# Kernel tuning notes

Hardware: AMD Instinct MI355X
Metric: run time of the kernel (lower is better)

## Reference

```python
import math
import jax, jax.numpy as jnp
import numpy as np

B, S, D, H, FF, N, V, C = 32, 512, 512, 8, 2048, 6, 32000, 16
EPS = 1e-6


def setup_inputs() -> dict:
    key = jax.random.key(0)
    c = [0]
    def w(shape, scale=0.02):
        c[0] += 1
        return jax.random.normal(jax.random.fold_in(key, c[0]), shape, jnp.float32) * scale
    inp = {}
    inp['src_emb'] = w((V, D)).at[0].set(0.0)  # padding_idx=0 row zeroed
    inp['tgt_emb'] = w((C, D)).at[0].set(0.0)
    for p in ['e', 'd', 's']:  # encoder self / decoder self / decoder cross attn
        for nm in ['wq', 'wk', 'wv', 'wo']:
            inp[f'{p}_{nm}'] = w((N, D, D))
            inp[f'{p}_{nm.replace("w", "b")}'] = w((N, D))
    for p in ['e', 'd']:
        inp[f'{p}_w1'] = w((N, D, FF)); inp[f'{p}_b1'] = w((N, FF))
        inp[f'{p}_w2'] = w((N, FF, D)); inp[f'{p}_b2'] = w((N, D))
    inp['gen_w'] = w((D * C, C)); inp['gen_b'] = w((C,))
    inp['scr_x'] = jax.random.randint(jax.random.fold_in(key, 999), (B, S), 0, V, dtype=jnp.int32)
    return inp


def _layernorm(x):
    # torch source: (x - mean) / (std + eps), std is unbiased (ddof=1); gamma=1, beta=0
    m = x.mean(-1, keepdims=True)
    s = jnp.std(x, axis=-1, keepdims=True, ddof=1)
    return (x - m) / (s + EPS)


def _mha(xq, xkv, wq, bq, wk, bk, wv, bv, wo, bo):
    b, lq, _ = xq.shape
    lk = xkv.shape[1]
    dk = D // H
    q = (xq @ wq + bq).reshape(b, lq, H, dk)
    k = (xkv @ wk + bk).reshape(b, lk, H, dk)
    v = (xkv @ wv + bv).reshape(b, lk, H, dk)
    scores = jnp.einsum('bqhd,bkhd->bhqk', q, k) / math.sqrt(dk)
    p = jax.nn.softmax(scores, axis=-1)
    o = jnp.einsum('bhqk,bkhd->bqhd', p, v).reshape(b, lq, D)
    return o @ wo + bo


def _ffn(x, w1, b1, w2, b2):
    return jax.nn.relu(x @ w1 + b1) @ w2 + b2


def _pos_encoding(L):
    pos = jnp.arange(L, dtype=jnp.float32)[:, None]
    div = jnp.exp(jnp.arange(0, D, 2, dtype=jnp.float32) * (-math.log(10000.0) / D))
    pe = jnp.zeros((L, D), jnp.float32)
    pe = pe.at[:, 0::2].set(jnp.sin(pos * div))
    pe = pe.at[:, 1::2].set(jnp.cos(pos * div))
    return pe


def reference(src_emb, tgt_emb,
              e_wq, e_bq, e_wk, e_bk, e_wv, e_bv, e_wo, e_bo, e_w1, e_b1, e_w2, e_b2,
              d_wq, d_bq, d_wk, d_bk, d_wv, d_bv, d_wo, d_bo,
              s_wq, s_bq, s_wk, s_bk, s_wv, s_bv, s_wo, s_bo,
              d_w1, d_b1, d_w2, d_b2, gen_w, gen_b, scr_x):
    sqrt_d = math.sqrt(D)
    # encoder
    x = src_emb[scr_x] * sqrt_d + _pos_encoding(S)[None]
    for i in range(N):
        t = _layernorm(x)
        x = x + _mha(t, t, e_wq[i], e_bq[i], e_wk[i], e_bk[i], e_wv[i], e_bv[i], e_wo[i], e_bo[i])
        t = _layernorm(x)
        x = x + _ffn(t, e_w1[i], e_b1[i], e_w2[i], e_b2[i])
    enc = _layernorm(x)
    # decoder over classify targets arange(C), repeated over batch
    y = jnp.broadcast_to(tgt_emb * sqrt_d + _pos_encoding(C), (B, C, D))
    for i in range(N):
        t = _layernorm(y)
        y = y + _mha(t, t, d_wq[i], d_bq[i], d_wk[i], d_bk[i], d_wv[i], d_bv[i], d_wo[i], d_bo[i])
        t = _layernorm(y)
        y = y + _mha(t, enc, s_wq[i], s_bq[i], s_wk[i], s_bk[i], s_wv[i], s_bv[i], s_wo[i], s_bo[i])
        t = _layernorm(y)
        y = y + _ffn(t, d_w1[i], d_b1[i], d_w2[i], d_b2[i])
    dec = _layernorm(y)
    logits = dec.reshape(B, -1) @ gen_w + gen_b
    return jax.nn.log_softmax(logits, axis=-1)
```

## Files before the change

kernel.cpp:

```cpp
#include <hip/hip_runtime.h>
#include <math.h>

#define NB  32
#define SS  512
#define DD  512
#define HH  8
#define FFD 2048
#define NLAY 6
#define CC  16
#define SQRTD 22.627416997969522f

typedef unsigned short u16;
typedef __attribute__((ext_vector_type(8))) short short8;
typedef __attribute__((ext_vector_type(8))) unsigned short u16x8;
typedef __attribute__((ext_vector_type(4))) float f32x4;

__device__ __forceinline__ u16 f2bf(float f) {
  unsigned u = __builtin_bit_cast(unsigned, f);
  u += 0x7fff + ((u >> 16) & 1);
  return (u16)(u >> 16);
}
__device__ __forceinline__ float bf2f(u16 u) {
  unsigned v = ((unsigned)u) << 16;
  return __builtin_bit_cast(float, v);
}
__device__ __forceinline__ void async16(const u16* g, u16* l) {
  __builtin_amdgcn_global_load_lds(
      (const __attribute__((address_space(1))) unsigned int*)g,
      (__attribute__((address_space(3))) unsigned int*)l, 16, 0, 0);
}
__device__ __forceinline__ int swz(int row, int slice) {
  return row * 128 + ((slice ^ (row & 7)) << 4);
}
__device__ __forceinline__ int vswz(int row, int slice) {
  return row * 128 + ((slice ^ (row & 7) ^ ((row >> 4) & 3)) << 4);
}

__device__ __forceinline__ float pe_val(int pos, int d) {
  int j = d >> 1;
  float freq = expf((float)j * -0.03597789207f);
  float ang = (float)pos * freq;
  return (d & 1) ? cosf(ang) : sinf(ang);
}

__global__ __launch_bounds__(512) void k_embed_src(
    const float* __restrict__ emb, const int* __restrict__ ids,
    float* __restrict__ x) {
  int tok = blockIdx.x;
  int d = threadIdx.x;
  int s = tok & (SS - 1);
  int id = ids[tok];
  x[(size_t)tok * DD + d] = emb[(size_t)id * DD + d] * SQRTD + pe_val(s, d);
}

__global__ __launch_bounds__(512) void k_embed_tgt(
    const float* __restrict__ emb, float* __restrict__ y) {
  int tok = blockIdx.x;
  int d = threadIdx.x;
  int c = tok & (CC - 1);
  y[(size_t)tok * DD + d] = emb[(size_t)c * DD + d] * SQRTD + pe_val(c, d);
}

template <typename OT>
__global__ __launch_bounds__(256) void k_layernorm(
    const float* __restrict__ X, OT* __restrict__ Y) {
  int row = blockIdx.x;
  int tid = threadIdx.x;
  int lane = tid & 63, wv = tid >> 6;
  const float* x = X + (size_t)row * DD;
  float2 v = *(const float2*)(x + tid * 2);
  float s = v.x + v.y;
  #pragma unroll
  for (int off = 32; off; off >>= 1) s += __shfl_xor(s, off);
  __shared__ float red[4];
  if (lane == 0) red[wv] = s;
  __syncthreads();
  float mean = (red[0] + red[1] + red[2] + red[3]) * (1.0f / DD);
  float dx = v.x - mean, dy = v.y - mean;
  float sq = dx * dx + dy * dy;
  #pragma unroll
  for (int off = 32; off; off >>= 1) sq += __shfl_xor(sq, off);
  __syncthreads();
  if (lane == 0) red[wv] = sq;
  __syncthreads();
  float var = (red[0] + red[1] + red[2] + red[3]) * (1.0f / (DD - 1));
  float inv = 1.0f / (sqrtf(var) + 1e-6f);
  float ox = dx * inv, oy = dy * inv;
  if constexpr (sizeof(OT) == 2) {
    ushort2 o; o.x = f2bf(ox); o.y = f2bf(oy);
    *(ushort2*)((u16*)Y + (size_t)row * DD + tid * 2) = o;
  } else {
    float2 o; o.x = ox; o.y = oy;
    *(float2*)((float*)Y + (size_t)row * DD + tid * 2) = o;
  }
}

__global__ __launch_bounds__(256) void k_wt(
    const float* __restrict__ in, u16* __restrict__ out, int K, int N,
    size_t ldl, int roff) {
  __shared__ float tile[32][33];
  const float* ip = in + (size_t)blockIdx.z * K * N;
  u16* op = out + (size_t)blockIdx.z * ldl;
  int n0 = blockIdx.x * 32, k0 = blockIdx.y * 32;
  int tx = threadIdx.x, ty = threadIdx.y;
  #pragma unroll
  for (int i = 0; i < 32; i += 8)
    tile[ty + i][tx] = ip[(size_t)(k0 + ty + i) * N + n0 + tx];
  __syncthreads();
  #pragma unroll
  for (int i = 0; i < 32; i += 8)
    op[(size_t)(roff + n0 + ty + i) * K + k0 + tx] = f2bf(tile[tx][ty + i]);
}

__global__ void k_bcat(const float* __restrict__ b0, const float* __restrict__ b1,
                       const float* __restrict__ b2, float* __restrict__ out,
                       int n0, int n1, int n2) {
  int lay = blockIdx.x, nt = n0 + n1 + n2;
  for (int t = threadIdx.x; t < nt; t += blockDim.x) {
    float v;
    if (t < n0) v = b0[(size_t)lay * n0 + t];
    else if (t < n0 + n1) v = b1[(size_t)lay * n1 + t - n0];
    else v = b2[(size_t)lay * n2 + t - n0 - n1];
    out[(size_t)lay * nt + t] = v;
  }
}

template <typename OT, bool RELU, bool RES, int NT>
__global__ __launch_bounds__(256) void k_mgemm(
    const u16* __restrict__ A, const u16* __restrict__ Bt,
    const float* __restrict__ bias, const float* __restrict__ res,
    OT* __restrict__ C, int M, int N, int K) {
  constexpr int MI = (NT == 128) ? 4 : 2;
  __shared__ u16 As[2][128 * 32];
  __shared__ u16 Bs[2][NT * 32];
  int nbn = N / NT;
  int cpx = gridDim.x >> 3;
  int bid = (blockIdx.x & 7) * cpx + (blockIdx.x >> 3);
  int bm = bid / nbn, bn = bid % nbn;
  int tid = threadIdx.x;
  int wid = tid >> 6, lane = tid & 63;
  int i0 = 2 * wid, i1 = 2 * wid + 1;
  int r0 = 16 * i0 + (lane >> 2), r1 = 16 * i1 + (lane >> 2);
  int kof = (lane & 3) * 8;
  const u16* Ag0 = A + (size_t)(bm * 128 + r0) * K + kof;
  const u16* Ag1 = A + (size_t)(bm * 128 + r1) * K + kof;
  const u16* Bg0;
  const u16* Bg1 = nullptr;
  if constexpr (NT == 128) {
    Bg0 = Bt + (size_t)(bn * 128 + r0) * K + kof;
    Bg1 = Bt + (size_t)(bn * 128 + r1) * K + kof;
  } else {
    int rb = 16 * wid + (lane >> 2);
    Bg0 = Bt + (size_t)(bn * 64 + rb) * K + kof;
  }
  f32x4 acc[MI][4] = {};
  int wm = wid >> 1, wn = wid & 1;
  int aoff, boff;
  if constexpr (NT == 128) {
    aoff = (wm * 64 + (lane & 15)) * 32 + (lane >> 4) * 8;
    boff = (wn * 64 + (lane & 15)) * 32 + (lane >> 4) * 8;
  } else {
    aoff = (wid * 32 + (lane & 15)) * 32 + (lane >> 4) * 8;
    boff = (lane & 15) * 32 + (lane >> 4) * 8;
  }

  auto stage = [&](int buf, int kel) {
    async16(Ag0 + kel, &As[buf][i0 * 512]);
    async16(Ag1 + kel, &As[buf][i1 * 512]);
    if constexpr (NT == 128) {
      async16(Bg0 + kel, &Bs[buf][i0 * 512]);
      async16(Bg1 + kel, &Bs[buf][i1 * 512]);
    } else {
      async16(Bg0 + kel, &Bs[buf][wid * 512]);
    }
  };

  stage(0, 0);
  __syncthreads();
  int nkt = K >> 5;
  for (int kt = 0; kt < nkt; ++kt) {
    int cur = kt & 1;
    if (kt + 1 < nkt) stage(cur ^ 1, (kt + 1) << 5);
    short8 af[MI], bfr[4];
    #pragma unroll
    for (int i = 0; i < MI; ++i)
      af[i] = *(const short8*)&As[cur][aoff + i * 16 * 32];
    #pragma unroll
    for (int i = 0; i < 4; ++i)
      bfr[i] = *(const short8*)&Bs[cur][boff + i * 16 * 32];
    #pragma unroll
    for (int mi = 0; mi < MI; ++mi)
      #pragma unroll
      for (int ni = 0; ni < 4; ++ni)
        acc[mi][ni] = __builtin_amdgcn_mfma_f32_16x16x32_bf16(
            af[mi], bfr[ni], acc[mi][ni], 0, 0, 0);
    __syncthreads();
  }

  int colb, rowb;
  if constexpr (NT == 128) {
    colb = bn * 128 + wn * 64 + (lane & 15);
    rowb = bm * 128 + wm * 64 + ((lane >> 4) << 2);
  } else {
    colb = bn * 64 + (lane & 15);
    rowb = bm * 128 + wid * 32 + ((lane >> 4) << 2);
  }
  #pragma unroll
  for (int mi = 0; mi < MI; ++mi)
    #pragma unroll
    for (int ni = 0; ni < 4; ++ni) {
      int col = colb + ni * 16;
      float bv = bias[col];
      #pragma unroll
      for (int r = 0; r < 4; ++r) {
        int row = rowb + mi * 16 + r;
        float v = acc[mi][ni][r] + bv;
        if constexpr (RES) v += res[(size_t)row * N + col];
        if constexpr (RELU) v = fmaxf(v, 0.f);
        if constexpr (sizeof(OT) == 2) ((u16*)C)[(size_t)row * N + col] = f2bf(v);
        else ((float*)C)[(size_t)row * N + col] = v;
      }
    }
}

__global__ __launch_bounds__(256) void k_attn3(
    const u16* __restrict__ Q, const u16* __restrict__ K,
    const u16* __restrict__ V, u16* __restrict__ O,
    int Lq, int Lk, int nqt, int ldq, int ldk, int ldv, int ldo) {
  __shared__ u16 Qs[64 * 64];
  __shared__ u16 Ks[64 * 64];
  __shared__ u16 VsT[64 * 64];
  __shared__ u16 Ps[64 * 64];
  int cpx = gridDim.x >> 3;
  int bid = (blockIdx.x & 7) * cpx + (blockIdx.x >> 3);
  int qt = bid % nqt;
  int bh = bid / nqt;
  int b = bh >> 3, h = bh & 7;
  int tid = threadIdx.x;
  int wv = tid >> 6, lane = tid & 63;
  int l16 = lane & 15, l4 = lane >> 4;
  int sr = tid >> 2;
  int sc2 = (tid & 3) << 1;

  {
    int qr = qt * 64 + sr;
    const u16* g = Q + (size_t)((size_t)b * Lq + qr) * ldq + h * 64 + (sc2 << 3);
    u16x8 v0 = *(const u16x8*)g;
    u16x8 v1 = *(const u16x8*)(g + 8);
    *(u16x8*)((char*)Qs + swz(sr, sc2)) = v0;
    *(u16x8*)((char*)Qs + swz(sr, sc2 + 1)) = v1;
  }

  f32x4 o_acc[4] = {};
  float l_r[4] = {0.f, 0.f, 0.f, 0.f};
  int qrow = wv * 16 + l16;

  int nkt = Lk >> 6;
  for (int kt = 0; kt < nkt; ++kt) {
    __syncthreads();
    {
      int kr = kt * 64 + sr;
      const u16* gk = K + (size_t)((size_t)b * Lk + kr) * ldk + h * 64 + (sc2 << 3);
      const u16* gv = V + (size_t)((size_t)b * Lk + kr) * ldv + h * 64 + (sc2 << 3);
      u16x8 k0 = *(const u16x8*)gk;
      u16x8 k1 = *(const u16x8*)(gk + 8);
      u16x8 vv0 = *(const u16x8*)gv;
      u16x8 vv1 = *(const u16x8*)(gv + 8);
      *(u16x8*)((char*)Ks + swz(sr, sc2)) = k0;
      *(u16x8*)((char*)Ks + swz(sr, sc2 + 1)) = k1;
      bool oddr = sr & 1;
      u16x8 send = oddr ? vv0 : vv1;
      int4 si = __builtin_bit_cast(int4, send);
      int4 ri;
      ri.x = __shfl_xor(si.x, 4); ri.y = __shfl_xor(si.y, 4);
      ri.z = __shfl_xor(si.z, 4); ri.w = __shfl_xor(si.w, 4);
      u16x8 recv = __builtin_bit_cast(u16x8, ri);
      int colbyte = (sr & 6) << 1;
      int slice = sr >> 3;
      int dbase = (sc2 << 3) + (oddr ? 8 : 0);
      #pragma unroll
      for (int j = 0; j < 8; ++j) {
        u16 lo = oddr ? recv[j] : vv0[j];
        u16 hi = oddr ? vv1[j] : recv[j];
        *(unsigned*)((char*)VsT + vswz(dbase + j, slice) + colbyte) =
            (unsigned)lo | ((unsigned)hi << 16);
      }
    }
    __syncthreads();

    short8 aQ0 = *(const short8*)((char*)Qs + swz(qrow, l4));
    short8 aQ1 = *(const short8*)((char*)Qs + swz(qrow, 4 + l4));
    f32x4 s_acc[4];
    #pragma unroll
    for (int ni = 0; ni < 4; ++ni) {
      int krow = ni * 16 + l16;
      short8 b0 = *(const short8*)((char*)Ks + swz(krow, l4));
      short8 b1 = *(const short8*)((char*)Ks + swz(krow, 4 + l4));
      f32x4 z = {};
      z = __builtin_amdgcn_mfma_f32_16x16x32_bf16(aQ0, b0, z, 0, 0, 0);
      z = __builtin_amdgcn_mfma_f32_16x16x32_bf16(aQ1, b1, z, 0, 0, 0);
      s_acc[ni] = z;
    }

    #pragma unroll
    for (int r = 0; r < 4; ++r) {
      int prow = wv * 16 + l4 * 4 + r;
      #pragma unroll
      for (int ni = 0; ni < 4; ++ni) {
        float p = __expf(s_acc[ni][r] * 0.125f);
        l_r[r] += p;
        int e = ni * 16 + l16;
        ((u16*)((char*)Ps + swz(prow, e >> 3)))[e & 7] = f2bf(p);
      }
    }

    short8 aP0 = *(const short8*)((char*)Ps + swz(qrow, l4));
    short8 aP1 = *(const short8*)((char*)Ps + swz(qrow, 4 + l4));
    #pragma unroll
    for (int ni = 0; ni < 4; ++ni) {
      int vrow = ni * 16 + l16;
      short8 b0 = *(const short8*)((char*)VsT + vswz(vrow, l4));
      short8 b1 = *(const short8*)((char*)VsT + vswz(vrow, 4 + l4));
      o_acc[ni] = __builtin_amdgcn_mfma_f32_16x16x32_bf16(aP0, b0, o_acc[ni], 0, 0, 0);
      o_acc[ni] = __builtin_amdgcn_mfma_f32_16x16x32_bf16(aP1, b1, o_acc[ni], 0, 0, 0);
    }
  }

  #pragma unroll
  for (int r = 0; r < 4; ++r)
    #pragma unroll
    for (int off = 8; off; off >>= 1) l_r[r] += __shfl_xor(l_r[r], off);

  #pragma unroll
  for (int r = 0; r < 4; ++r) {
    int q = qt * 64 + wv * 16 + l4 * 4 + r;
    float inv = 1.0f / l_r[r];
    u16* op = O + (size_t)((size_t)b * Lq + q) * ldo + h * 64 + l16;
    #pragma unroll
    for (int ni = 0; ni < 4; ++ni)
      op[ni * 16] = f2bf(o_acc[ni][r] * inv);
  }
}

__global__ __launch_bounds__(256) void k_attn4(
    const u16* __restrict__ Q, const u16* __restrict__ K,
    const u16* __restrict__ V, u16* __restrict__ O,
    int Lk, int ldq, int ldk, int ldv, int ldo) {
  __shared__ u16 Qs[16 * 64];
  __shared__ u16 Ks[4][64 * 64];
  __shared__ u16 VsT[4][64 * 64];
  __shared__ u16 Ps[4][16 * 64];
  int cpx = gridDim.x >> 3;
  int bid = (blockIdx.x & 7) * cpx + (blockIdx.x >> 3);
  int b = bid >> 3, h = bid & 7;
  int tid = threadIdx.x;
  int wv = tid >> 6, lane = tid & 63;
  int l16 = lane & 15, l4 = lane >> 4;

  if (tid < 64) {
    int qr = tid >> 2;
    int sc2 = (tid & 3) << 1;
    const u16* g = Q + (size_t)((size_t)b * CC + qr) * ldq + h * 64 + (sc2 << 3);
    u16x8 v0 = *(const u16x8*)g;
    u16x8 v1 = *(const u16x8*)(g + 8);
    *(u16x8*)((char*)Qs + swz(qr, sc2)) = v0;
    *(u16x8*)((char*)Qs + swz(qr, sc2 + 1)) = v1;
  }
  __syncthreads();

  u16* KsW = Ks[wv];
  u16* VsW = VsT[wv];
  u16* PsW = Ps[wv];

  f32x4 o_acc[4] = {};
  float l_r[4] = {0.f, 0.f, 0.f, 0.f};

  int nkt = (Lk + 63) >> 6;
  for (int kt = wv; kt < nkt; kt += 4) {
    int kr = kt * 64 + lane; if (kr >= Lk) kr = Lk - 1;
    const u16* gk = K + (size_t)((size_t)b * Lk + kr) * ldk + h * 64;
    const u16* gv = V + (size_t)((size_t)b * Lk + kr) * ldv + h * 64;
    u16x8 vvv[8];
    #pragma unroll
    for (int c = 0; c < 8; ++c) {
      u16x8 kk = *(const u16x8*)(gk + c * 8);
      *(u16x8*)((char*)KsW + swz(lane, c)) = kk;
      vvv[c] = *(const u16x8*)(gv + c * 8);
    }
    bool oddr = lane & 1;
    int4 s0 = __builtin_bit_cast(int4, oddr ? vvv[0] : vvv[4]);
    int4 s1 = __builtin_bit_cast(int4, oddr ? vvv[1] : vvv[5]);
    int4 s2 = __builtin_bit_cast(int4, oddr ? vvv[2] : vvv[6]);
    int4 s3 = __builtin_bit_cast(int4, oddr ? vvv[3] : vvv[7]);
    int4 r0, r1, r2, r3;
    r0.x = __shfl_xor(s0.x, 1); r0.y = __shfl_xor(s0.y, 1);
    r0.z = __shfl_xor(s0.z, 1); r0.w = __shfl_xor(s0.w, 1);
    r1.x = __shfl_xor(s1.x, 1); r1.y = __shfl_xor(s1.y, 1);
    r1.z = __shfl_xor(s1.z, 1); r1.w = __shfl_xor(s1.w, 1);
    r2.x = __shfl_xor(s2.x, 1); r2.y = __shfl_xor(s2.y, 1);
    r2.z = __shfl_xor(s2.z, 1); r2.w = __shfl_xor(s2.w, 1);
    r3.x = __shfl_xor(s3.x, 1); r3.y = __shfl_xor(s3.y, 1);
    r3.z = __shfl_xor(s3.z, 1); r3.w = __shfl_xor(s3.w, 1);
    u16x8 rcv[4] = {
      __builtin_bit_cast(u16x8, r0), __builtin_bit_cast(u16x8, r1),
      __builtin_bit_cast(u16x8, r2), __builtin_bit_cast(u16x8, r3)};
    int colbyte = (lane & 6) << 1;
    int slice = lane >> 3;
    int dbase = oddr ? 32 : 0;
    #pragma unroll
    for (int c = 0; c < 4; ++c)
      #pragma unroll
      for (int j = 0; j < 8; ++j) {
        int d = dbase + c * 8 + j;
        u16 lo = oddr ? rcv[c][j] : vvv[c][j];
        u16 hi = oddr ? vvv[4 + c][j] : rcv[c][j];
        *(unsigned*)((char*)VsW + vswz(d, slice) + colbyte) =
            (unsigned)lo | ((unsigned)hi << 16);
      }

    short8 aQ0 = *(const short8*)((char*)Qs + swz(l16, l4));
    short8 aQ1 = *(const short8*)((char*)Qs + swz(l16, 4 + l4));
    f32x4 s_acc[4];
    __builtin_amdgcn_s_setprio(1);
    #pragma unroll
    for (int ni = 0; ni < 4; ++ni) {
      int krow = ni * 16 + l16;
      short8 b0 = *(const short8*)((char*)KsW + swz(krow, l4));
      short8 b1 = *(const short8*)((char*)KsW + swz(krow, 4 + l4));
      f32x4 z = {};
      z = __builtin_amdgcn_mfma_f32_16x16x32_bf16(aQ0, b0, z, 0, 0, 0);
      z = __builtin_amdgcn_mfma_f32_16x16x32_bf16(aQ1, b1, z, 0, 0, 0);
      s_acc[ni] = z;
    }
    __builtin_amdgcn_s_setprio(0);

    #pragma unroll
    for (int r = 0; r < 4; ++r) {
      int prow = l4 * 4 + r;
      #pragma unroll
      for (int ni = 0; ni < 4; ++ni) {
        int kg = kt * 64 + ni * 16 + l16;
        float p = (kg < Lk) ? __expf(s_acc[ni][r] * 0.125f) : 0.f;
        l_r[r] += p;
        int e = ni * 16 + l16;
        ((u16*)((char*)PsW + swz(prow, e >> 3)))[e & 7] = f2bf(p);
      }
    }

    short8 aP0 = *(const short8*)((char*)PsW + swz(l16, l4));
    short8 aP1 = *(const short8*)((char*)PsW + swz(l16, 4 + l4));
    __builtin_amdgcn_s_setprio(1);
    #pragma unroll
    for (int ni = 0; ni < 4; ++ni) {
      int vrow = ni * 16 + l16;
      short8 b0 = *(const short8*)((char*)VsW + vswz(vrow, l4));
      short8 b1 = *(const short8*)((char*)VsW + vswz(vrow, 4 + l4));
      o_acc[ni] = __builtin_amdgcn_mfma_f32_16x16x32_bf16(aP0, b0, o_acc[ni], 0, 0, 0);
      o_acc[ni] = __builtin_amdgcn_mfma_f32_16x16x32_bf16(aP1, b1, o_acc[ni], 0, 0, 0);
    }
    __builtin_amdgcn_s_setprio(0);
  }

  #pragma unroll
  for (int r = 0; r < 4; ++r)
    #pragma unroll
    for (int off = 8; off; off >>= 1) l_r[r] += __shfl_xor(l_r[r], off);

  float* cO = (float*)KsW;
  float* cL = (float*)VsW;
  #pragma unroll
  for (int r = 0; r < 4; ++r) {
    int q = l4 * 4 + r;
    if (l16 == 0) cL[q] = l_r[r];
    #pragma unroll
    for (int ni = 0; ni < 4; ++ni)
      cO[q * 64 + ni * 16 + l16] = o_acc[ni][r];
  }
  __syncthreads();

  #pragma unroll
  for (int i = 0; i < 4; ++i) {
    int e = tid + 256 * i;
    int q = e >> 6, d = e & 63;
    float den = 0.f, num = 0.f;
    #pragma unroll
    for (int w = 0; w < 4; ++w) {
      den += ((float*)VsT[w])[q];
      num += ((float*)Ks[w])[q * 64 + d];
    }
    O[(size_t)((size_t)b * CC + q) * ldo + h * 64 + d] = f2bf(num / den);
  }
}

__global__ __launch_bounds__(256) void k_gen(
    const float* __restrict__ dec, const float* __restrict__ Wg,
    const float* __restrict__ bg, float* __restrict__ out) {
  int b = blockIdx.x;
  int t = threadIdx.x;
  int n = t & 15, ch = t >> 4;
  const float* a = dec + (size_t)b * (CC * DD);
  float p = 0.f;
  int k0 = ch * 512;
  for (int kk = k0; kk < k0 + 512; ++kk) p += a[kk] * Wg[(size_t)kk * CC + n];
  __shared__ float red[16][17];
  red[ch][n] = p;
  __syncthreads();
  __shared__ float ls[16];
  __shared__ float mm[2];
  if (t < 16) {
    float sv = bg[t];
    #pragma unroll
    for (int jj = 0; jj < 16; ++jj) sv += red[jj][t];
    ls[t] = sv;
  }
  __syncthreads();
  if (t == 0) {
    float m = ls[0];
    for (int jj = 1; jj < 16; ++jj) m = fmaxf(m, ls[jj]);
    float se = 0.f;
    for (int jj = 0; jj < 16; ++jj) se += expf(ls[jj] - m);
    mm[0] = m; mm[1] = logf(se);
  }
  __syncthreads();
  if (t < 16) out[(size_t)b * CC + t] = ls[t] - mm[0] - mm[1];
}

extern "C" void kernel_launch(void* const* d_in, const int* in_sizes, int n_in,
                              void* d_out, int out_size, void* d_ws, size_t ws_size,
                              hipStream_t stream) {
  (void)in_sizes; (void)n_in; (void)out_size; (void)ws_size;
  const float* src_emb = (const float*)d_in[0];
  const float* tgt_emb = (const float*)d_in[1];
  const float* e_wq = (const float*)d_in[2];
  const float* e_bq = (const float*)d_in[3];
  const float* e_wk = (const float*)d_in[4];
  const float* e_bk = (const float*)d_in[5];
  const float* e_wv = (const float*)d_in[6];
  const float* e_bv = (const float*)d_in[7];
  const float* e_wo = (const float*)d_in[8];
  const float* e_bo = (const float*)d_in[9];
  const float* d_wq = (const float*)d_in[10];
  const float* d_bq = (const float*)d_in[11];
  const float* d_wk = (const float*)d_in[12];
  const float* d_bk = (const float*)d_in[13];
  const float* d_wv = (const float*)d_in[14];
  const float* d_bv = (const float*)d_in[15];
  const float* d_wo = (const float*)d_in[16];
  const float* d_bo = (const float*)d_in[17];
  const float* s_wq = (const float*)d_in[18];
  const float* s_bq = (const float*)d_in[19];
  const float* s_wk = (const float*)d_in[20];
  const float* s_bk = (const float*)d_in[21];
  const float* s_wv = (const float*)d_in[22];
  const float* s_bv = (const float*)d_in[23];
  const float* s_wo = (const float*)d_in[24];
  const float* s_bo = (const float*)d_in[25];
  const float* e_w1 = (const float*)d_in[26];
  const float* e_b1 = (const float*)d_in[27];
  const float* e_w2 = (const float*)d_in[28];
  const float* e_b2 = (const float*)d_in[29];
  const float* dw1  = (const float*)d_in[30];
  const float* db1  = (const float*)d_in[31];
  const float* dw2  = (const float*)d_in[32];
  const float* db2  = (const float*)d_in[33];
  const float* gen_w = (const float*)d_in[34];
  const float* gen_b = (const float*)d_in[35];
  const int*   scr   = (const int*)d_in[36];

  float* ws = (float*)d_ws;
  const size_t NBS = (size_t)NB * SS * DD;
  const size_t BCD = (size_t)NB * CC * DD;
  float* x    = ws;
  u16*  t_bf  = (u16*)(ws + NBS);
  u16*  enc_bf = t_bf;
  float* dsm  = ws + NBS + NBS / 2;
  float* dy   = dsm;
  float* tdf  = dsm + BCD;
  u16*  td_bf = (u16*)(tdf + BCD);
  u16*  aod_bf = td_bf + BCD;
  u16*  dqkv_act = aod_bf + BCD;
  u16*  middd_bf = dqkv_act + 3 * BCD;
  u16*  eqkv_act = (u16*)(ws + 2 * NBS);
  u16*  midd_e   = eqkv_act;
  u16*  kv_big   = eqkv_act;
  u16*  kv_x     = (u16*)x;
  u16* wp = (u16*)(ws + 4 * NBS);
  const size_t SQKV = (size_t)NLAY * 1536 * 512;
  const size_t SDD  = (size_t)NLAY * 512 * 512;
  const size_t SKV  = (size_t)NLAY * 1024 * 512;
  const size_t SFF  = (size_t)NLAY * 2048 * 512;
  u16* eqkv_t = wp;            wp += SQKV;
  u16* ewo_t  = wp;            wp += SDD;
  u16* ew1_t  = wp;            wp += SFF;
  u16* ew2_t  = wp;            wp += SFF;
  u16* dqkv_t = wp;            wp += SQKV;
  u16* dwo_t  = wp;            wp += SDD;
  u16* sq_t   = wp;            wp += SDD;
  u16* skv_t  = wp;            wp += SKV;
  u16* swo_t  = wp;            wp += SDD;
  u16* dw1_t  = wp;            wp += SFF;
  u16* dw2_t  = wp;            wp += SFF;
  float* ebqkv = (float*)wp;
  float* dbqkv = ebqkv + NLAY * 1536;
  float* sbkv  = dbqkv + NLAY * 1536;

  const int BS = NB * SS;
  const int BC = NB * CC;

  auto wt = [&](const float* in, u16* out, int K, int N, size_t ldl, int roff) {
    k_wt<<<dim3(N / 32, K / 32, NLAY), dim3(32, 8), 0, stream>>>(in, out, K, N, ldl, roff);
  };
  auto mg = [&](const u16* A, const u16* Bt, const float* bias,
                const float* res, void* C, int M, int N, int K, int relu, int obf) {
    int g128 = (M / 128) * (N / 128);
    if (g128 >= 1024) {
      dim3 g(g128);
      if (obf) {
        if (relu) k_mgemm<u16, true, false, 128><<<g, 256, 0, stream>>>(A, Bt, bias, nullptr, (u16*)C, M, N, K);
        else      k_mgemm<u16, false, false, 128><<<g, 256, 0, stream>>>(A, Bt, bias, nullptr, (u16*)C, M, N, K);
      } else {
        if (res)  k_mgemm<float, false, true, 128><<<g, 256, 0, stream>>>(A, Bt, bias, res, (float*)C, M, N, K);
        else      k_mgemm<float, false, false, 128><<<g, 256, 0, stream>>>(A, Bt, bias, nullptr, (float*)C, M, N, K);
      }
    } else {
      dim3 g((M / 128) * (N / 64));
      if (obf) {
        if (relu) k_mgemm<u16, true, false, 64><<<g, 256, 0, stream>>>(A, Bt, bias, nullptr, (u16*)C, M, N, K);
        else      k_mgemm<u16, false, false, 64><<<g, 256, 0, stream>>>(A, Bt, bias, nullptr, (u16*)C, M, N, K);
      } else {
        if (res)  k_mgemm<float, false, true, 64><<<g, 256, 0, stream>>>(A, Bt, bias, res, (float*)C, M, N, K);
        else      k_mgemm<float, false, false, 64><<<g, 256, 0, stream>>>(A, Bt, bias, nullptr, (float*)C, M, N, K);
      }
    }
  };

  wt(e_wq, eqkv_t, 512, 512, 1536 * 512, 0);
  wt(e_wk, eqkv_t, 512, 512, 1536 * 512, 512);
  wt(e_wv, eqkv_t, 512, 512, 1536 * 512, 1024);
  wt(e_wo, ewo_t,  512, 512, 512 * 512, 0);
  wt(e_w1, ew1_t,  512, 2048, 2048 * 512, 0);
  wt(e_w2, ew2_t,  2048, 512, (size_t)512 * 2048, 0);
  wt(d_wq, dqkv_t, 512, 512, 1536 * 512, 0);
  wt(d_wk, dqkv_t, 512, 512, 1536 * 512, 512);
  wt(d_wv, dqkv_t, 512, 512, 1536 * 512, 1024);
  wt(d_wo, dwo_t,  512, 512, 512 * 512, 0);
  wt(s_wq, sq_t,   512, 512, 512 * 512, 0);
  wt(s_wk, skv_t,  512, 512, 1024 * 512, 0);
  wt(s_wv, skv_t,  512, 512, 1024 * 512, 512);
  wt(s_wo, swo_t,  512, 512, 512 * 512, 0);
  wt(dw1,  dw1_t,  512, 2048, 2048 * 512, 0);
  wt(dw2,  dw2_t,  2048, 512, (size_t)512 * 2048, 0);
  k_bcat<<<NLAY, 512, 0, stream>>>(e_bq, e_bk, e_bv, ebqkv, 512, 512, 512);
  k_bcat<<<NLAY, 512, 0, stream>>>(d_bq, d_bk, d_bv, dbqkv, 512, 512, 512);
  k_bcat<<<NLAY, 512, 0, stream>>>(s_bk, s_bv, s_bv, sbkv, 512, 512, 0);

  k_embed_src<<<BS, 512, 0, stream>>>(src_emb, scr, x);
  for (int i = 0; i < NLAY; ++i) {
    size_t bo = (size_t)i * DD, b1o = (size_t)i * FFD;
    k_layernorm<u16><<<BS, 256, 0, stream>>>(x, t_bf);
    mg(t_bf, eqkv_t + (size_t)i * 1536 * 512, ebqkv + i * 1536, nullptr,
       eqkv_act, BS, 1536, 512, 0, 1);
    k_attn3<<<NB * HH * (SS / 64), 256, 0, stream>>>(
        eqkv_act, eqkv_act + 512, eqkv_act + 1024, t_bf,
        SS, SS, SS / 64, 1536, 1536, 1536, 512);
    mg(t_bf, ewo_t + (size_t)i * 512 * 512, e_bo + bo, x, x, BS, 512, 512, 0, 0);
    k_layernorm<u16><<<BS, 256, 0, stream>>>(x, t_bf);
    mg(t_bf, ew1_t + (size_t)i * 2048 * 512, e_b1 + b1o, nullptr,
       midd_e, BS, 2048, 512, 1, 1);
    mg(midd_e, ew2_t + (size_t)i * 512 * 2048, e_b2 + bo, x, x, BS, 512, 2048, 0, 0);
  }
  k_layernorm<u16><<<BS, 256, 0, stream>>>(x, enc_bf);

  mg(enc_bf, skv_t, sbkv, nullptr, kv_big, BS, 2048, 512, 0, 1);
  mg(enc_bf, skv_t + (size_t)2 * 1024 * 512, sbkv + 2 * 1024, nullptr,
     kv_x, BS, 1024, 512, 0, 1);

  k_embed_tgt<<<BC, 512, 0, stream>>>(tgt_emb, dy);
  for (int i = 0; i < NLAY; ++i) {
    size_t bo = (size_t)i * DD, b1o = (size_t)i * FFD;
    if (i == 2)
      mg(enc_bf, skv_t + (size_t)3 * 1024 * 512, sbkv + 3 * 1024, nullptr,
         kv_big, BS, 2048, 512, 0, 1);
    if (i == 3)
      mg(enc_bf, skv_t + (size_t)5 * 1024 * 512, sbkv + 5 * 1024, nullptr,
         kv_x, BS, 1024, 512, 0, 1);
    k_layernorm<u16><<<BC, 256, 0, stream>>>(dy, td_bf);
    mg(td_bf, dqkv_t + (size_t)i * 1536 * 512, dbqkv + i * 1536, nullptr,
       dqkv_act, BC, 1536, 512, 0, 1);
    k_attn4<<<NB * HH, 256, 0, stream>>>(
        dqkv_act, dqkv_act + 512, dqkv_act + 1024, aod_bf,
        CC, 1536, 1536, 1536, 512);
    mg(aod_bf, dwo_t + (size_t)i * 512 * 512, d_bo + bo, dy, dy, BC, 512, 512, 0, 0);
    k_layernorm<u16><<<BC, 256, 0, stream>>>(dy, td_bf);
    mg(td_bf, sq_t + (size_t)i * 512 * 512, s_bq + bo, nullptr,
       dqkv_act, BC, 512, 512, 0, 1);
    const u16* kvp; int ldkv;
    if (i < 2)      { kvp = kv_big + i * 1024;        ldkv = 2048; }
    else if (i == 2){ kvp = kv_x;                     ldkv = 1024; }
    else if (i < 5) { kvp = kv_big + (i - 3) * 1024;  ldkv = 2048; }
    else            { kvp = kv_x;                     ldkv = 1024; }
    k_attn4<<<NB * HH, 256, 0, stream>>>(
        dqkv_act, kvp, kvp + 512, aod_bf,
        SS, 512, ldkv, ldkv, 512);
    mg(aod_bf, swo_t + (size_t)i * 512 * 512, s_bo + bo, dy, dy, BC, 512, 512, 0, 0);
    k_layernorm<u16><<<BC, 256, 0, stream>>>(dy, td_bf);
    mg(td_bf, dw1_t + (size_t)i * 2048 * 512, db1 + b1o, nullptr,
       middd_bf, BC, 2048, 512, 1, 1);
    mg(middd_bf, dw2_t + (size_t)i * 512 * 2048, db2 + bo, dy, dy, BC, 512, 2048, 0, 0);
  }
  k_layernorm<float><<<BC, 256, 0, stream>>>(dy, tdf);
  k_gen<<<NB, 256, 0, stream>>>(tdf, gen_w, gen_b, (float*)d_out);
}
```

Measured before the change: 2.401 ms.

## Process 128 query rows per encoder attention block to reuse K/V tiles

The encoder attention kernel now handles 128 query rows per block instead of 64, with each wave computing two 16-row fragments against every loaded K/V tile. The grid shrinks by half, so each K/V tile load and transpose serves twice as many queries. This cuts global K/V traffic and shared-memory staging per query, at the cost of doubled accumulator registers and larger LDS for Q and P, which may lower occupancy. The grid drops to 1024 blocks, still several per CU.

Measured after the change: 2.405 ms. No clear change (+0.2%).

```diff
diff --git a/kernel.cpp b/kernel.cpp
--- a/kernel.cpp
+++ b/kernel.cpp
@@ -227,10 +227,10 @@
     const u16* __restrict__ Q, const u16* __restrict__ K,
     const u16* __restrict__ V, u16* __restrict__ O,
     int Lq, int Lk, int nqt, int ldq, int ldk, int ldv, int ldo) {
-  __shared__ u16 Qs[64 * 64];
+  __shared__ u16 Qs[128 * 64];
   __shared__ u16 Ks[64 * 64];
   __shared__ u16 VsT[64 * 64];
-  __shared__ u16 Ps[64 * 64];
+  __shared__ u16 Ps[128 * 64];
   int cpx = gridDim.x >> 3;
   int bid = (blockIdx.x & 7) * cpx + (blockIdx.x >> 3);
   int qt = bid % nqt;
@@ -242,19 +242,19 @@
   int sr = tid >> 2;
   int sc2 = (tid & 3) << 1;
 
-  {
-    int qr = qt * 64 + sr;
+  #pragma unroll
+  for (int half = 0; half < 2; ++half) {
+    int lrow = sr + 64 * half;
+    int qr = qt * 128 + lrow;
     const u16* g = Q + (size_t)((size_t)b * Lq + qr) * ldq + h * 64 + (sc2 << 3);
     u16x8 v0 = *(const u16x8*)g;
     u16x8 v1 = *(const u16x8*)(g + 8);
-    *(u16x8*)((char*)Qs + swz(sr, sc2)) = v0;
-    *(u16x8*)((char*)Qs + swz(sr, sc2 + 1)) = v1;
-  }
-
-  f32x4 o_acc[4] = {};
-  float l_r[4] = {0.f, 0.f, 0.f, 0.f};
-  int qrow = wv * 16 + l16;
-
+    *(u16x8*)((char*)Qs + swz(lrow, sc2)) = v0;
+    *(u16x8*)((char*)Qs + swz(lrow, sc2 + 1)) = v1;
+  }
+
+  f32x4 o_acc[2][4] = {};
+  float l_r[2][4] = {};
   int nkt = Lk >> 6;
   for (int kt = 0; kt < nkt; ++kt) {
     __syncthreads();
@@ -288,58 +288,66 @@
     }
     __syncthreads();
 
-    short8 aQ0 = *(const short8*)((char*)Qs + swz(qrow, l4));
-    short8 aQ1 = *(const short8*)((char*)Qs + swz(qrow, 4 + l4));
-    f32x4 s_acc[4];
-    #pragma unroll
-    for (int ni = 0; ni < 4; ++ni) {
-      int krow = ni * 16 + l16;
-      short8 b0 = *(const short8*)((char*)Ks + swz(krow, l4));
-      short8 b1 = *(const short8*)((char*)Ks + swz(krow, 4 + l4));
-      f32x4 z = {};
-      z = __builtin_amdgcn_mfma_f32_16x16x32_bf16(aQ0, b0, z, 0, 0, 0);
-      z = __builtin_amdgcn_mfma_f32_16x16x32_bf16(aQ1, b1, z, 0, 0, 0);
-      s_acc[ni] = z;
-    }
-
+    #pragma unroll
+    for (int f = 0; f < 2; ++f) {
+      int qrow = wv * 32 + f * 16 + l16;
+      short8 aQ0 = *(const short8*)((char*)Qs + swz(qrow, l4));
+      short8 aQ1 = *(const short8*)((char*)Qs + swz(qrow, 4 + l4));
+      f32x4 s_acc[4];
+      #pragma unroll
+      for (int ni = 0; ni < 4; ++ni) {
+        int krow = ni * 16 + l16;
+        short8 b0 = *(const short8*)((char*)Ks + swz(krow, l4));
+        short8 b1 = *(const short8*)((char*)Ks + swz(krow, 4 + l4));
+        f32x4 z = {};
+        z = __builtin_amdgcn_mfma_f32_16x16x32_bf16(aQ0, b0, z, 0, 0, 0);
+        z = __builtin_amdgcn_mfma_f32_16x16x32_bf16(aQ1, b1, z, 0, 0, 0);
+        s_acc[ni] = z;
+      }
+
+      #pragma unroll
+      for (int r = 0; r < 4; ++r) {
+        int prow = wv * 32 + f * 16 + l4 * 4 + r;
+        #pragma unroll
+        for (int ni = 0; ni < 4; ++ni) {
+          float p = __expf(s_acc[ni][r] * 0.125f);
+          l_r[f][r] += p;
+          int e = ni * 16 + l16;
+          ((u16*)((char*)Ps + swz(prow, e >> 3)))[e & 7] = f2bf(p);
+        }
+      }
+
+      short8 aP0 = *(const short8*)((char*)Ps + swz(qrow, l4));
+      short8 aP1 = *(const short8*)((char*)Ps + swz(qrow, 4 + l4));
+      #pragma unroll
+      for (int ni = 0; ni < 4; ++ni) {
+        int vrow = ni * 16 + l16;
+        short8 b0 = *(const short8*)((char*)VsT + vswz(vrow, l4));
+        short8 b1 = *(const short8*)((char*)VsT + vswz(vrow, 4 + l4));
+        o_acc[f][ni] = __builtin_amdgcn_mfma_f32_16x16x32_bf16(aP0, b0, o_acc[f][ni], 0, 0, 0);
+        o_acc[f][ni] = __builtin_amdgcn_mfma_f32_16x16x32_bf16(aP1, b1, o_acc[f][ni], 0, 0, 0);
+      }
+    }
+  }
+
+  #pragma unroll
+  for (int f = 0; f < 2; ++f)
+    #pragma unroll
+    for (int r = 0; r < 4; ++r)
+      #pragma unroll
+      for (int off = 8; off; off >>= 1) l_r[f][r] += __shfl_xor(l_r[f][r], off);
+
+  #pragma unroll
+  for (int f = 0; f < 2; ++f)
     #pragma unroll
     for (int r = 0; r < 4; ++r) {
-      int prow = wv * 16 + l4 * 4 + r;
-      #pragma unroll
-      for (int ni = 0; ni < 4; ++ni) {
-        float p = __expf(s_acc[ni][r] * 0.125f);
-        l_r[r] += p;
-        int e = ni * 16 + l16;
-        ((u16*)((char*)Ps + swz(prow, e >> 3)))[e & 7] = f2bf(p);
-      }
-    }
-
-    short8 aP0 = *(const short8*)((char*)Ps + swz(qrow, l4));
-    short8 aP1 = *(const short8*)((char*)Ps + swz(qrow, 4 + l4));
-    #pragma unroll
-    for (int ni = 0; ni < 4; ++ni) {
-      int vrow = ni * 16 + l16;
-      short8 b0 = *(const short8*)((char*)VsT + vswz(vrow, l4));
-      short8 b1 = *(const short8*)((char*)VsT + vswz(vrow, 4 + l4));
-      o_acc[ni] = __builtin_amdgcn_mfma_f32_16x16x32_bf16(aP0, b0, o_acc[ni], 0, 0, 0);
-      o_acc[ni] = __builtin_amdgcn_mfma_f32_16x16x32_bf16(aP1, b1, o_acc[ni], 0, 0, 0);
-    }
-  }
-
-  #pragma unroll
-  for (int r = 0; r < 4; ++r)
-    #pragma unroll
-    for (int off = 8; off; off >>= 1) l_r[r] += __shfl_xor(l_r[r], off);
-
-  #pragma unroll
-  for (int r = 0; r < 4; ++r) {
-    int q = qt * 64 + wv * 16 + l4 * 4 + r;
-    float inv = 1.0f / l_r[r];
-    u16* op = O + (size_t)((size_t)b * Lq + q) * ldo + h * 64 + l16;
-    #pragma unroll
-    for (int ni = 0; ni < 4; ++ni)
-      op[ni * 16] = f2bf(o_acc[ni][r] * inv);
-  }
+      int q = qt * 128 + wv * 32 + f * 16 + l4 * 4 + r;
+      float inv = 1.0f / l_r[f][r];
+      u16* op = O + (size_t)((size_t)b * Lq + q) * ldo + h * 64 + l16;
+      #pragma unroll
+      for (int ni = 0; ni < 4; ++ni)
+        op[ni * 16] = f2bf(o_acc[f][ni][r] * inv);
+    }
 }
 
 __global__ __launch_bounds__(256) void k_attn4(
@@ -660,9 +668,9 @@
     k_layernorm<u16><<<BS, 256, 0, stream>>>(x, t_bf);
     mg(t_bf, eqkv_t + (size_t)i * 1536 * 512, ebqkv + i * 1536, nullptr,
        eqkv_act, BS, 1536, 512, 0, 1);
-    k_attn3<<<NB * HH * (SS / 64), 256, 0, stream>>>(
+    k_attn3<<<NB * HH * (SS / 128), 256, 0, stream>>>(
         eqkv_act, eqkv_act + 512, eqkv_act + 1024, t_bf,
-        SS, SS, SS / 64, 1536, 1536, 1536, 512);
+        SS, SS, SS / 128, 1536, 1536, 1536, 512);
     mg(t_bf, ewo_t + (size_t)i * 512 * 512, e_bo + bo, x, x, BS, 512, 512, 0, 0);
     k_layernorm<u16><<<BS, 256, 0, stream>>>(x, t_bf);
     mg(t_bf, ew1_t + (size_t)i * 2048 * 512, e_b1 + b1o, nullptr,
```
